# Kernel tuning notes

Hardware: AMD Instinct MI355X
Metric: run time of the kernel (lower is better)

The kernel has to match this reference:

```python
import jax, jax.numpy as jnp
import numpy as np

USER_NUM = 100000
ITEM_NUM = 100000
N_NODES = USER_NUM + ITEM_NUM
EMB_DIM = 64
N_LAYERS = 3
NNZ = 6400000


def setup_inputs() -> dict:
    key = jax.random.key(0)
    k1, k2, k3, k4, k5 = jax.random.split(key, 5)
    # Xavier-normal-ish embedding tables
    user_emb = jax.random.normal(k1, (USER_NUM, EMB_DIM), dtype=jnp.float32) * 0.05
    item_emb = jax.random.normal(k2, (ITEM_NUM, EMB_DIM), dtype=jnp.float32) * 0.05
    # Sparse hypergraph in COO form: out[dst] += val * x[src]
    edge_src = jax.random.randint(k3, (NNZ,), 0, N_NODES, dtype=jnp.int32)
    edge_dst = jax.random.randint(k4, (NNZ,), 0, N_NODES, dtype=jnp.int32)
    edge_val = jax.random.uniform(k5, (NNZ,), dtype=jnp.float32) / 32.0  # ~normalized adj values
    return {"user_emb": user_emb, "item_emb": item_emb, "edge_val": edge_val,
            "edge_src": edge_src, "edge_dst": edge_dst}


def _spmm(edge_src, edge_dst, edge_val, x):
    # y = A @ x with A in COO form: gather rows, scale, scatter-add.
    msgs = x[edge_src] * edge_val[:, None]           # [nnz, D]
    return jax.ops.segment_sum(msgs, edge_dst, num_segments=N_NODES)


def reference(user_emb, item_emb, edge_val, edge_src, edge_dst):
    ego = jnp.concatenate([user_emb, item_emb], axis=0)  # [N, D]
    all_embeddings = [ego]
    for _ in range(N_LAYERS):
        ego = _spmm(edge_src, edge_dst, edge_val, ego)
        all_embeddings.append(ego)
    all_emb = jnp.concatenate(all_embeddings, axis=1)    # [N, D*(L+1)]
    u_g = all_emb[:USER_NUM, :]
    i_g = all_emb[USER_NUM:, :]
    return (u_g, i_g)
```

## Files before the change

### kernel.cpp

```cpp
#include <hip/hip_runtime.h>
#include <hip/hip_fp16.h>
#include <stdint.h>

#define U_NUM   100000
#define NNODES  200000
#define DIM     64
#define OUTDIM  256
#define NNZ     6400000

#define BSHIFT  6
#define BNODES  64
#define NB      (NNODES >> BSHIFT)
#define BCAP    4096
#define NBLK    256
#define EPB     (NNZ / NBLK)

#define WS_ROWEND    0
#define WS_PAIRS     800000
#define WS_BCNT      52000000
#define WS_PART      52012500
#define WS_NEEDED_NEW ((size_t)WS_PART + (size_t)NBLK * NB * 4)
#define WS_MIR0      55220000
#define WS_MIR1      (WS_MIR0 + (size_t)NNODES * DIM * 2)
#define WS_NEEDED_H  (WS_MIR1 + (size_t)NNODES * DIM * 2)
#define WS_NEEDED_OLD (800000 + (size_t)NNZ * 8)

__global__ void init_out(const float* __restrict__ user_emb,
                         const float* __restrict__ item_emb,
                         float* __restrict__ out) {
    int t = blockIdx.x * blockDim.x + threadIdx.x;
    if (t >= NNODES * 16) return;
    int n = t >> 4;
    int c = (t & 15) << 2;
    const float* s = (n < U_NUM) ? (user_emb + (size_t)n * DIM + c)
                                 : (item_emb + (size_t)(n - U_NUM) * DIM + c);
    *(float4*)(out + (size_t)n * OUTDIM + c) = *(const float4*)s;
}

__global__ void init_out_h(const float* __restrict__ user_emb,
                           const float* __restrict__ item_emb,
                           float* __restrict__ out,
                           __half* __restrict__ mir) {
    int t = blockIdx.x * blockDim.x + threadIdx.x;
    if (t >= NNODES * 16) return;
    int n = t >> 4;
    int c = (t & 15) << 2;
    const float* s = (n < U_NUM) ? (user_emb + (size_t)n * DIM + c)
                                 : (item_emb + (size_t)(n - U_NUM) * DIM + c);
    float4 v = *(const float4*)s;
    *(float4*)(out + (size_t)n * OUTDIM + c) = v;
    __half2 h01 = __floats2half2_rn(v.x, v.y);
    __half2 h23 = __floats2half2_rn(v.z, v.w);
    uint2 u;
    u.x = *(uint32_t*)&h01;
    u.y = *(uint32_t*)&h23;
    *(uint2*)(mir + (size_t)n * DIM + c) = u;
}


__global__ __launch_bounds__(1024) void bucket_hist(const int* __restrict__ edst,
                                                    uint32_t* __restrict__ partials) {
    __shared__ uint32_t h[NB];
    for (int i = threadIdx.x; i < NB; i += 1024) h[i] = 0u;
    __syncthreads();
    int blk = blockIdx.x;
    int e0 = blk * EPB;
    for (int i = threadIdx.x; i < EPB; i += 1024)
        atomicAdd(&h[(uint32_t)edst[e0 + i] >> BSHIFT], 1u);
    __syncthreads();
    for (int i = threadIdx.x; i < NB; i += 1024)
        partials[(size_t)blk * NB + i] = h[i];
}

__global__ void bucket_colsum(const uint32_t* __restrict__ partials,
                              uint32_t* __restrict__ bcnt) {
    int b = blockIdx.x * blockDim.x + threadIdx.x;
    if (b >= NB) return;
    uint32_t s = 0u;
    for (int blk = 0; blk < NBLK; ++blk) s += partials[(size_t)blk * NB + b];
    bcnt[b] = s;
}

__global__ __launch_bounds__(1024) void scan_bcnt(uint32_t* __restrict__ cnt) {
    __shared__ uint32_t lds[1024];
    __shared__ uint32_t s_carry;
    int t = threadIdx.x;
    if (t == 0) s_carry = 0u;
    __syncthreads();
    for (int base = 0; base < NB; base += 1024) {
        int i = base + t;
        uint32_t v = (i < NB) ? cnt[i] : 0u;
        lds[t] = v;
        __syncthreads();
        for (int off = 1; off < 1024; off <<= 1) {
            uint32_t add = (t >= off) ? lds[t - off] : 0u;
            __syncthreads();
            lds[t] += add;
            __syncthreads();
        }
        uint32_t incl  = lds[t];
        uint32_t total = lds[1023];
        uint32_t c     = s_carry;
        __syncthreads();
        if (i < NB) cnt[i] = incl - v + c;
        if (t == 0) s_carry = c + total;
        __syncthreads();
    }
}

__global__ void bucket_offsets(uint32_t* __restrict__ partials,
                               const uint32_t* __restrict__ bstart) {
    int b = blockIdx.x * blockDim.x + threadIdx.x;
    if (b >= NB) return;
    uint32_t run = bstart[b];
    for (int blk = 0; blk < NBLK; ++blk) {
        size_t idx = (size_t)blk * NB + b;
        uint32_t t = partials[idx];
        partials[idx] = run;
        run += t;
    }
}

__global__ __launch_bounds__(1024) void scatter_buckets(const int*   __restrict__ esrc,
                                                        const int*   __restrict__ edst,
                                                        const float* __restrict__ eval,
                                                        const uint32_t* __restrict__ partials,
                                                        int2* __restrict__ pairs) {
    __shared__ uint32_t cur[NB];
    int blk = blockIdx.x;
    for (int i = threadIdx.x; i < NB; i += 1024)
        cur[i] = partials[(size_t)blk * NB + i];
    __syncthreads();
    int e0 = blk * EPB;
    for (int i = threadIdx.x; i < EPB; i += 1024) {
        int e = e0 + i;
        int d = edst[e];
        int b = (uint32_t)d >> BSHIFT;
        uint32_t pos = atomicAdd(&cur[b], 1u);
        int packed = esrc[e] | ((d & (BNODES - 1)) << 18);
        pairs[pos] = make_int2(packed, __float_as_int(eval[e]));
    }
}

__global__ __launch_bounds__(256) void bucket_sort(const uint32_t* __restrict__ bstart_arr,
                                                   int2* __restrict__ pairs,
                                                   uint32_t* __restrict__ rowend) {
    __shared__ int2 ebuf[BCAP];
    __shared__ uint32_t scnt[BNODES];
    int b = blockIdx.x;
    uint32_t start = bstart_arr[b];
    uint32_t end   = (b == NB - 1) ? (uint32_t)NNZ : bstart_arr[b + 1];
    int n = (int)(end - start);
    if (n > BCAP) n = BCAP;
    if (threadIdx.x < BNODES) scnt[threadIdx.x] = 0u;
    __syncthreads();
    for (int i = threadIdx.x; i < n; i += 256) {
        int2 e = pairs[start + i];
        ebuf[i] = e;
        atomicAdd(&scnt[(uint32_t)e.x >> 18], 1u);
    }
    __syncthreads();
    if (threadIdx.x < 64) {
        uint32_t c = scnt[threadIdx.x];
        uint32_t v = c;
        for (int off = 1; off < 64; off <<= 1) {
            uint32_t nv = __shfl_up(v, (unsigned)off, 64);
            if ((int)threadIdx.x >= off) v += nv;
        }
        rowend[b * BNODES + threadIdx.x] = start + v;
        scnt[threadIdx.x] = v - c;
    }
    __syncthreads();
    for (int i = threadIdx.x; i < n; i += 256) {
        int2 e = ebuf[i];
        int dlow = (uint32_t)e.x >> 18;
        uint32_t pos = start + atomicAdd(&scnt[dlow], 1u);
        pairs[pos] = make_int2(e.x & 0x3FFFF, e.y);
    }
}


__global__ __launch_bounds__(256) void spmm_gather_h(const uint32_t* __restrict__ rowend,
                                                     const int2*     __restrict__ pairs,
                                                     const __half*   __restrict__ mirp,
                                                     float*          __restrict__ cur,
                                                     __half*         __restrict__ mirc) {
    int w    = (blockIdx.x * blockDim.x + threadIdx.x) >> 6;
    int lane = threadIdx.x & 63;
    if (w >= NNODES) return;
    uint32_t start = (w == 0) ? 0u : rowend[w - 1];
    uint32_t end   = rowend[w];
    float acc = 0.f;
    uint32_t i = start;
    for (; i + 4 <= end; i += 4) {
        int2 p0 = pairs[i + 0];
        int2 p1 = pairs[i + 1];
        int2 p2 = pairs[i + 2];
        int2 p3 = pairs[i + 3];
        float x0 = __half2float(mirp[(size_t)p0.x * DIM + lane]);
        float x1 = __half2float(mirp[(size_t)p1.x * DIM + lane]);
        float x2 = __half2float(mirp[(size_t)p2.x * DIM + lane]);
        float x3 = __half2float(mirp[(size_t)p3.x * DIM + lane]);
        acc = fmaf(x0, __int_as_float(p0.y), acc);
        acc = fmaf(x1, __int_as_float(p1.y), acc);
        acc = fmaf(x2, __int_as_float(p2.y), acc);
        acc = fmaf(x3, __int_as_float(p3.y), acc);
    }
    for (; i < end; ++i) {
        int2 p = pairs[i];
        acc = fmaf(__half2float(mirp[(size_t)p.x * DIM + lane]), __int_as_float(p.y), acc);
    }
    cur[(size_t)w * OUTDIM + lane] = acc;
    if (mirc) mirc[(size_t)w * DIM + lane] = __float2half(acc);
}

__global__ __launch_bounds__(256) void spmm_gather(const uint32_t* __restrict__ rowend,
                                                   const int2*     __restrict__ pairs,
                                                   const float*    __restrict__ prev,
                                                   float*          __restrict__ cur) {
    int w    = (blockIdx.x * blockDim.x + threadIdx.x) >> 6;
    int lane = threadIdx.x & 63;
    if (w >= NNODES) return;
    uint32_t start = (w == 0) ? 0u : rowend[w - 1];
    uint32_t end   = rowend[w];
    float acc = 0.f;
    uint32_t i = start;
    for (; i + 4 <= end; i += 4) {
        int2 p0 = pairs[i + 0];
        int2 p1 = pairs[i + 1];
        int2 p2 = pairs[i + 2];
        int2 p3 = pairs[i + 3];
        float x0 = prev[(size_t)p0.x * OUTDIM + lane];
        float x1 = prev[(size_t)p1.x * OUTDIM + lane];
        float x2 = prev[(size_t)p2.x * OUTDIM + lane];
        float x3 = prev[(size_t)p3.x * OUTDIM + lane];
        acc = fmaf(x0, __int_as_float(p0.y), acc);
        acc = fmaf(x1, __int_as_float(p1.y), acc);
        acc = fmaf(x2, __int_as_float(p2.y), acc);
        acc = fmaf(x3, __int_as_float(p3.y), acc);
    }
    for (; i < end; ++i) {
        int2 p = pairs[i];
        acc = fmaf(prev[(size_t)p.x * OUTDIM + lane], __int_as_float(p.y), acc);
    }
    cur[(size_t)w * OUTDIM + lane] = acc;
}


__global__ void zero_cnt(uint32_t* __restrict__ cnt) {
    int t = blockIdx.x * blockDim.x + threadIdx.x;
    if (t < NNODES) cnt[t] = 0u;
}

__global__ void hist(const int* __restrict__ edst, uint32_t* __restrict__ cnt) {
    int e = blockIdx.x * blockDim.x + threadIdx.x;
    if (e < NNZ) atomicAdd(&cnt[edst[e]], 1u);
}

__global__ __launch_bounds__(1024) void scan_cnt(uint32_t* __restrict__ cnt) {
    __shared__ uint32_t lds[1024];
    __shared__ uint32_t s_carry;
    int t = threadIdx.x;
    if (t == 0) s_carry = 0u;
    __syncthreads();
    for (int base = 0; base < NNODES; base += 1024) {
        int i = base + t;
        uint32_t v = (i < NNODES) ? cnt[i] : 0u;
        lds[t] = v;
        __syncthreads();
        for (int off = 1; off < 1024; off <<= 1) {
            uint32_t add = (t >= off) ? lds[t - off] : 0u;
            __syncthreads();
            lds[t] += add;
            __syncthreads();
        }
        uint32_t incl  = lds[t];
        uint32_t total = lds[1023];
        uint32_t c     = s_carry;
        __syncthreads();
        if (i < NNODES) cnt[i] = incl - v + c;
        if (t == 0) s_carry = c + total;
        __syncthreads();
    }
}

__global__ void fill_pairs(const int*   __restrict__ esrc,
                           const int*   __restrict__ edst,
                           const float* __restrict__ eval,
                           uint32_t*    __restrict__ cnt,
                           int2*        __restrict__ pairs) {
    int e = blockIdx.x * blockDim.x + threadIdx.x;
    if (e >= NNZ) return;
    int d = edst[e];
    uint32_t pos = atomicAdd(&cnt[d], 1u);
    pairs[pos] = make_int2(esrc[e], __float_as_int(eval[e]));
}

__global__ void init_out_full(const float* __restrict__ user_emb,
                              const float* __restrict__ item_emb,
                              float* __restrict__ out) {
    int t = blockIdx.x * blockDim.x + threadIdx.x;
    if (t >= NNODES * 64) return;
    int n = t >> 6;
    int c = (t & 63) << 2;
    float4 v = make_float4(0.f, 0.f, 0.f, 0.f);
    if (c < DIM) {
        const float* s = (n < U_NUM) ? (user_emb + (size_t)n * DIM + c)
                                     : (item_emb + (size_t)(n - U_NUM) * DIM + c);
        v = *(const float4*)s;
    }
    *(float4*)(out + (size_t)n * OUTDIM + c) = v;
}

__global__ void scatter_spmm(const int*   __restrict__ esrc,
                             const int*   __restrict__ edst,
                             const float* __restrict__ eval,
                             const float* __restrict__ prev,
                             float*       __restrict__ cur) {
    int t = blockIdx.x * blockDim.x + threadIdx.x;
    if (t >= NNZ * 16) return;
    int e = t >> 4;
    int j = (t & 15) << 2;
    int s = esrc[e];
    int d = edst[e];
    float v = eval[e];
    float4 x = *(const float4*)(prev + (size_t)s * OUTDIM + j);
    float* ap = cur + (size_t)d * OUTDIM + j;
    unsafeAtomicAdd(ap + 0, x.x * v);
    unsafeAtomicAdd(ap + 1, x.y * v);
    unsafeAtomicAdd(ap + 2, x.z * v);
    unsafeAtomicAdd(ap + 3, x.w * v);
}

extern "C" void kernel_launch(void* const* d_in, const int* in_sizes, int n_in,
                              void* d_out, int out_size, void* d_ws, size_t ws_size,
                              hipStream_t stream) {
    const float* user_emb = (const float*)d_in[0];
    const float* item_emb = (const float*)d_in[1];
    const float* eval     = (const float*)d_in[2];
    const int*   esrc     = (const int*)d_in[3];
    const int*   edst     = (const int*)d_in[4];
    float* out = (float*)d_out;

    if (ws_size >= WS_NEEDED_H) {
        uint32_t* rowend   = (uint32_t*)((char*)d_ws + WS_ROWEND);
        int2*     pairs    = (int2*)   ((char*)d_ws + WS_PAIRS);
        uint32_t* bcnt     = (uint32_t*)((char*)d_ws + WS_BCNT);
        uint32_t* partials = (uint32_t*)((char*)d_ws + WS_PART);
        __half*   mir0     = (__half*) ((char*)d_ws + WS_MIR0);
        __half*   mir1     = (__half*) ((char*)d_ws + WS_MIR1);

        init_out_h<<<(NNODES * 16 + 255) / 256, 256, 0, stream>>>(user_emb, item_emb, out, mir0);
        bucket_hist<<<NBLK, 1024, 0, stream>>>(edst, partials);
        bucket_colsum<<<(NB + 255) / 256, 256, 0, stream>>>(partials, bcnt);
        scan_bcnt<<<1, 1024, 0, stream>>>(bcnt);
        bucket_offsets<<<(NB + 255) / 256, 256, 0, stream>>>(partials, bcnt);
        scatter_buckets<<<NBLK, 1024, 0, stream>>>(esrc, edst, eval, partials, pairs);
        bucket_sort<<<NB, 256, 0, stream>>>(bcnt, pairs, rowend);

        spmm_gather_h<<<(NNODES * 64) / 256, 256, 0, stream>>>(
            rowend, pairs, mir0, out + (size_t)1 * DIM, mir1);
        spmm_gather_h<<<(NNODES * 64) / 256, 256, 0, stream>>>(
            rowend, pairs, mir1, out + (size_t)2 * DIM, mir0);
        spmm_gather_h<<<(NNODES * 64) / 256, 256, 0, stream>>>(
            rowend, pairs, mir0, out + (size_t)3 * DIM, (__half*)nullptr);
    } else if (ws_size >= WS_NEEDED_NEW) {
        uint32_t* rowend   = (uint32_t*)((char*)d_ws + WS_ROWEND);
        int2*     pairs    = (int2*)   ((char*)d_ws + WS_PAIRS);
        uint32_t* bcnt     = (uint32_t*)((char*)d_ws + WS_BCNT);
        uint32_t* partials = (uint32_t*)((char*)d_ws + WS_PART);

        init_out<<<(NNODES * 16 + 255) / 256, 256, 0, stream>>>(user_emb, item_emb, out);
        bucket_hist<<<NBLK, 1024, 0, stream>>>(edst, partials);
        bucket_colsum<<<(NB + 255) / 256, 256, 0, stream>>>(partials, bcnt);
        scan_bcnt<<<1, 1024, 0, stream>>>(bcnt);
        bucket_offsets<<<(NB + 255) / 256, 256, 0, stream>>>(partials, bcnt);
        scatter_buckets<<<NBLK, 1024, 0, stream>>>(esrc, edst, eval, partials, pairs);
        bucket_sort<<<NB, 256, 0, stream>>>(bcnt, pairs, rowend);

        for (int l = 1; l <= 3; ++l) {
            spmm_gather<<<(NNODES * 64) / 256, 256, 0, stream>>>(
                rowend, pairs,
                out + (size_t)(l - 1) * DIM,
                out + (size_t)l * DIM);
        }
    } else if (ws_size >= WS_NEEDED_OLD) {
        uint32_t* cnt   = (uint32_t*)d_ws;
        int2*     pairs = (int2*)((char*)d_ws + 800000);

        init_out<<<(NNODES * 16 + 255) / 256, 256, 0, stream>>>(user_emb, item_emb, out);
        zero_cnt<<<(NNODES + 255) / 256, 256, 0, stream>>>(cnt);
        hist<<<NNZ / 256, 256, 0, stream>>>(edst, cnt);
        scan_cnt<<<1, 1024, 0, stream>>>(cnt);
        fill_pairs<<<NNZ / 256, 256, 0, stream>>>(esrc, edst, eval, cnt, pairs);

        for (int l = 1; l <= 3; ++l) {
            spmm_gather<<<(NNODES * 64) / 256, 256, 0, stream>>>(
                cnt, pairs,
                out + (size_t)(l - 1) * DIM,
                out + (size_t)l * DIM);
        }
    } else {
        init_out_full<<<(NNODES * 64 + 255) / 256, 256, 0, stream>>>(user_emb, item_emb, out);
        for (int l = 1; l <= 3; ++l) {
            scatter_spmm<<<(NNZ * 16) / 256, 256, 0, stream>>>(
                esrc, edst, eval,
                out + (size_t)(l - 1) * DIM,
                out + (size_t)l * DIM);
        }
    }
}
```

Before: 1.246 ms.

## Process eight edges per wavefront iteration with 16-byte half row loads

```diff
diff --git a/kernel.cpp b/kernel.cpp
--- a/kernel.cpp
+++ b/kernel.cpp
@@ -180,38 +180,75 @@
 }
 
 
-__global__ __launch_bounds__(256) void spmm_gather_h(const uint32_t* __restrict__ rowend,
-                                                     const int2*     __restrict__ pairs,
-                                                     const __half*   __restrict__ mirp,
-                                                     float*          __restrict__ cur,
-                                                     __half*         __restrict__ mirc) {
+__global__ __launch_bounds__(256) void spmm_gather_h8(const uint32_t* __restrict__ rowend,
+                                                      const int2*     __restrict__ pairs,
+                                                      const __half*   __restrict__ mirp,
+                                                      float*          __restrict__ cur,
+                                                      __half*         __restrict__ mirc) {
     int w    = (blockIdx.x * blockDim.x + threadIdx.x) >> 6;
     int lane = threadIdx.x & 63;
     if (w >= NNODES) return;
     uint32_t start = (w == 0) ? 0u : rowend[w - 1];
     uint32_t end   = rowend[w];
-    float acc = 0.f;
-    uint32_t i = start;
-    for (; i + 4 <= end; i += 4) {
-        int2 p0 = pairs[i + 0];
-        int2 p1 = pairs[i + 1];
-        int2 p2 = pairs[i + 2];
-        int2 p3 = pairs[i + 3];
-        float x0 = __half2float(mirp[(size_t)p0.x * DIM + lane]);
-        float x1 = __half2float(mirp[(size_t)p1.x * DIM + lane]);
-        float x2 = __half2float(mirp[(size_t)p2.x * DIM + lane]);
-        float x3 = __half2float(mirp[(size_t)p3.x * DIM + lane]);
-        acc = fmaf(x0, __int_as_float(p0.y), acc);
-        acc = fmaf(x1, __int_as_float(p1.y), acc);
-        acc = fmaf(x2, __int_as_float(p2.y), acc);
-        acc = fmaf(x3, __int_as_float(p3.y), acc);
-    }
-    for (; i < end; ++i) {
-        int2 p = pairs[i];
-        acc = fmaf(__half2float(mirp[(size_t)p.x * DIM + lane]), __int_as_float(p.y), acc);
-    }
-    cur[(size_t)w * OUTDIM + lane] = acc;
-    if (mirc) mirc[(size_t)w * DIM + lane] = __float2half(acc);
+    int g = lane >> 3;
+    int l = lane & 7;
+
+    float acc0 = 0.f, acc1 = 0.f, acc2 = 0.f, acc3 = 0.f;
+    float acc4 = 0.f, acc5 = 0.f, acc6 = 0.f, acc7 = 0.f;
+
+    for (uint32_t i = start; i < end; i += 8) {
+        uint32_t idx = i + (uint32_t)g;
+        int2 p = (idx < end) ? pairs[idx] : make_int2(0, 0);
+        const uint4* rp = (const uint4*)(mirp + (size_t)p.x * DIM) + l;
+        uint4 hv = *rp;
+        float v = __int_as_float(p.y);
+        __half2 h0 = *(__half2*)&hv.x;
+        __half2 h1 = *(__half2*)&hv.y;
+        __half2 h2 = *(__half2*)&hv.z;
+        __half2 h3 = *(__half2*)&hv.w;
+        float2 f0 = __half22float2(h0);
+        float2 f1 = __half22float2(h1);
+        float2 f2 = __half22float2(h2);
+        float2 f3 = __half22float2(h3);
+        acc0 = fmaf(f0.x, v, acc0);
+        acc1 = fmaf(f0.y, v, acc1);
+        acc2 = fmaf(f1.x, v, acc2);
+        acc3 = fmaf(f1.y, v, acc3);
+        acc4 = fmaf(f2.x, v, acc4);
+        acc5 = fmaf(f2.y, v, acc5);
+        acc6 = fmaf(f3.x, v, acc6);
+        acc7 = fmaf(f3.y, v, acc7);
+    }
+
+    #pragma unroll
+    for (int off = 8; off < 64; off <<= 1) {
+        acc0 += __shfl_xor(acc0, off, 64);
+        acc1 += __shfl_xor(acc1, off, 64);
+        acc2 += __shfl_xor(acc2, off, 64);
+        acc3 += __shfl_xor(acc3, off, 64);
+        acc4 += __shfl_xor(acc4, off, 64);
+        acc5 += __shfl_xor(acc5, off, 64);
+        acc6 += __shfl_xor(acc6, off, 64);
+        acc7 += __shfl_xor(acc7, off, 64);
+    }
+
+    if (lane < 8) {
+        float* op = cur + (size_t)w * OUTDIM + 8 * l;
+        *(float4*)(op + 0) = make_float4(acc0, acc1, acc2, acc3);
+        *(float4*)(op + 4) = make_float4(acc4, acc5, acc6, acc7);
+        if (mirc) {
+            __half2 a0 = __floats2half2_rn(acc0, acc1);
+            __half2 a1 = __floats2half2_rn(acc2, acc3);
+            __half2 a2 = __floats2half2_rn(acc4, acc5);
+            __half2 a3 = __floats2half2_rn(acc6, acc7);
+            uint4 u;
+            u.x = *(uint32_t*)&a0;
+            u.y = *(uint32_t*)&a1;
+            u.z = *(uint32_t*)&a2;
+            u.w = *(uint32_t*)&a3;
+            *(uint4*)(mirc + (size_t)w * DIM + 8 * l) = u;
+        }
+    }
 }
 
 __global__ __launch_bounds__(256) void spmm_gather(const uint32_t* __restrict__ rowend,
@@ -358,11 +395,11 @@
         scatter_buckets<<<NBLK, 1024, 0, stream>>>(esrc, edst, eval, partials, pairs);
         bucket_sort<<<NB, 256, 0, stream>>>(bcnt, pairs, rowend);
 
-        spmm_gather_h<<<(NNODES * 64) / 256, 256, 0, stream>>>(
+        spmm_gather_h8<<<(NNODES * 64) / 256, 256, 0, stream>>>(
             rowend, pairs, mir0, out + (size_t)1 * DIM, mir1);
-        spmm_gather_h<<<(NNODES * 64) / 256, 256, 0, stream>>>(
+        spmm_gather_h8<<<(NNODES * 64) / 256, 256, 0, stream>>>(
             rowend, pairs, mir1, out + (size_t)2 * DIM, mir0);
-        spmm_gather_h<<<(NNODES * 64) / 256, 256, 0, stream>>>(
+        spmm_gather_h8<<<(NNODES * 64) / 256, 256, 0, stream>>>(
             rowend, pairs, mir0, out + (size_t)3 * DIM, (__half*)nullptr);
     } else if (ws_size >= WS_NEEDED_NEW) {
         uint32_t* rowend   = (uint32_t*)((char*)d_ws + WS_ROWEND);
```

Measured after the change: 1.093 ms. 12.2% less time.
